# Performance work log

Measured on AMD Instinct MI355X. Metric: run time of the kernel, lower is better.

Reference implementation:

```python
import jax, jax.numpy as jnp
import numpy as np

LN_EPS = 1e-5

def _pos_enc(S, d):
    # sinusoid table; row 0 is all zeros (matches position_encoding_init)
    j = np.arange(d)
    pos = np.arange(S, dtype=np.float64)[:, None]
    pe = pos / np.power(10000.0, 2 * (j // 2) / d)
    pe[0, :] = 0.0
    pe[1:, 0::2] = np.sin(pe[1:, 0::2])
    pe[1:, 1::2] = np.cos(pe[1:, 1::2])
    return jnp.asarray(pe, dtype=jnp.float32)


def setup_inputs() -> dict:
    key = jax.random.key(0)
    ks = jax.random.split(key, 8)
    B, S, din, dhid = 8, 2048, 1024, 1024
    inp = jax.random.normal(ks[0], (B, S, din), dtype=jnp.float32)
    lens = jax.random.randint(ks[1], (B,), 1, S, dtype=jnp.int64)
    scale = 0.02
    Wq = jax.random.normal(ks[2], (2 * din, dhid), dtype=jnp.float32) * scale
    Wk = jax.random.normal(ks[3], (2 * din, dhid), dtype=jnp.float32) * scale
    Wv = jax.random.normal(ks[4], (2 * din, dhid), dtype=jnp.float32) * scale
    bq = jax.random.normal(ks[5], (dhid,), dtype=jnp.float32) * scale
    bk = jax.random.normal(ks[6], (dhid,), dtype=jnp.float32) * scale
    bv = jax.random.normal(ks[7], (dhid,), dtype=jnp.float32) * scale
    gamma = jnp.ones((dhid,), dtype=jnp.float32)
    beta = jnp.zeros((dhid,), dtype=jnp.float32)
    return {"inp": inp, "Wq": Wq, "bq": bq, "Wk": Wk, "bk": bk,
            "Wv": Wv, "bv": bv, "gamma": gamma, "beta": beta, "lens": lens}


def reference(inp, Wq, bq, Wk, bk, Wv, bv, gamma, beta, lens):
    B, S, d = inp.shape
    pe = _pos_enc(S, d)  # [S, d], static given shapes
    x = jnp.concatenate([inp, jnp.broadcast_to(pe, (B, S, d))], axis=-1)  # [B,S,2d]
    q = x @ Wq + bq  # [B,S,dk]
    k = x @ Wk + bk
    v = x @ Wv + bv
    scores = jnp.einsum('bqd,bkd->bqk', q, k)  # [B,S,S]
    # NOTE: softmax over the QUERY axis (dim=1), then post-hoc scale, as in the source
    attn = jax.nn.softmax(scores, axis=1) / jnp.sqrt(jnp.asarray(q.shape[-1], jnp.float32))
    sa = jnp.einsum('bqk,bkd->bqd', attn, v)  # [B,S,dv]
    mu = sa.mean(axis=-1, keepdims=True)
    var = sa.var(axis=-1, keepdims=True)
    ln = (sa - mu) / jnp.sqrt(var + LN_EPS) * gamma + beta
    context = ln.sum(axis=1) / S  # [B,dv]
    return (sa, context)
```

## Files before the change

kernel.cpp:

```cpp
#include <hip/hip_runtime.h>
#include <math.h>

#define B_   8
#define S_   2048
#define D_   1024
#define M_   (B_ * S_)
#define K2_  (2 * D_)


__global__ __launch_bounds__(256) void pe_fill(float* __restrict__ pe) {
    const int s  = blockIdx.x;
    const int j0 = threadIdx.x * 4;
#pragma unroll
    for (int e = 0; e < 4; ++e) {
        int j = j0 + e;
        double ex = (double)(2 * (j >> 1)) / (double)D_;
        double dv = pow(10000.0, ex);
        double a  = (double)s / dv;
        float val;
        if (s == 0) val = 0.0f;
        else        val = (j & 1) ? (float)cos(a) : (float)sin(a);
        pe[s * D_ + j] = val;
    }
}


__device__ __forceinline__ void stage_trans(const float* __restrict__ src,
                                            int ld, int row0, int k0,
                                            float (*T)[132], int tid) {
#pragma unroll
    for (int it = 0; it < 2; ++it) {
        int f  = tid + it * 256;
        int r  = f >> 2;
        int c4 = (f & 3) << 2;
        float4 v = *(const float4*)&src[(size_t)(row0 + r) * ld + k0 + c4];
        T[c4 + 0][r] = v.x;
        T[c4 + 1][r] = v.y;
        T[c4 + 2][r] = v.z;
        T[c4 + 3][r] = v.w;
    }
}

__device__ __forceinline__ void stage_direct(const float* __restrict__ src,
                                             int ld, int k0, int col0,
                                             float (*T)[132], int tid) {
#pragma unroll
    for (int it = 0; it < 2; ++it) {
        int f  = tid + it * 256;
        int kr = f >> 5;
        int c4 = (f & 31) << 2;
        float4 v = *(const float4*)&src[(size_t)(k0 + kr) * ld + col0 + c4];
        *(float4*)&T[kr][c4] = v;
    }
}

__device__ __forceinline__ void mm_core(const float (*As)[132],
                                        const float (*Bs)[132],
                                        float acc[8][8], int tx, int ty) {
#pragma unroll
    for (int kk = 0; kk < 16; ++kk) {
        float a[8], b[8];
        *(float4*)&a[0] = *(const float4*)&As[kk][ty * 8];
        *(float4*)&a[4] = *(const float4*)&As[kk][ty * 8 + 4];
        *(float4*)&b[0] = *(const float4*)&Bs[kk][tx * 8];
        *(float4*)&b[4] = *(const float4*)&Bs[kk][tx * 8 + 4];
#pragma unroll
        for (int i = 0; i < 8; ++i)
#pragma unroll
            for (int j = 0; j < 8; ++j)
                acc[i][j] = fmaf(a[i], b[j], acc[i][j]);
    }
}

__global__ __launch_bounds__(256) void proj_gemm(
        const float* __restrict__ inp, const float* __restrict__ pe,
        const float* __restrict__ W, const float* __restrict__ bias,
        float* __restrict__ out, int m_base) {
    __shared__ float As[16][132];
    __shared__ float Bs[16][132];
    const int tid = threadIdx.x;
    const int tx = tid & 15, ty = tid >> 4;
    const int m0 = blockIdx.x * 128;
    const int n0 = blockIdx.y * 128;

    float acc[8][8];
#pragma unroll
    for (int i = 0; i < 8; ++i)
#pragma unroll
        for (int j = 0; j < 8; ++j) acc[i][j] = 0.0f;

    for (int k0 = 0; k0 < K2_; k0 += 16) {
#pragma unroll
        for (int it = 0; it < 2; ++it) {
            int f  = tid + it * 256;
            int r  = f >> 2;
            int c4 = (f & 3) << 2;
            int gm = m_base + m0 + r;
            float4 v;
            if (k0 < D_) {
                v = *(const float4*)&inp[(size_t)gm * D_ + k0 + c4];
            } else {
                int s = gm & (S_ - 1);
                v = *(const float4*)&pe[(size_t)s * D_ + (k0 - D_) + c4];
            }
            As[c4 + 0][r] = v.x;
            As[c4 + 1][r] = v.y;
            As[c4 + 2][r] = v.z;
            As[c4 + 3][r] = v.w;
        }
        stage_direct(W, D_, k0, n0, Bs, tid);
        __syncthreads();
        mm_core(As, Bs, acc, tx, ty);
        __syncthreads();
    }

    float bv[8];
    *(float4*)&bv[0] = *(const float4*)&bias[n0 + tx * 8];
    *(float4*)&bv[4] = *(const float4*)&bias[n0 + tx * 8 + 4];
#pragma unroll
    for (int i = 0; i < 8; ++i) {
        int m = m0 + ty * 8 + i;
        float o[8];
#pragma unroll
        for (int j = 0; j < 8; ++j) o[j] = acc[i][j] + bv[j];
        *(float4*)&out[(size_t)m * D_ + n0 + tx * 8]     = *(float4*)&o[0];
        *(float4*)&out[(size_t)m * D_ + n0 + tx * 8 + 4] = *(float4*)&o[4];
    }
}

__global__ __launch_bounds__(256) void qk_gemm(
        const float* __restrict__ q, const float* __restrict__ k,
        float* __restrict__ scoresT) {
    __shared__ float As[16][132];
    __shared__ float Bs[16][132];
    const int tid = threadIdx.x;
    const int tx = tid & 15, ty = tid >> 4;
    const int b  = blockIdx.z;
    const int i0 = blockIdx.x * 128;
    const int j0 = blockIdx.y * 128;
    const float* Kb = k + (size_t)b * S_ * D_;
    const float* Qb = q + (size_t)b * S_ * D_;

    float acc[8][8];
#pragma unroll
    for (int i = 0; i < 8; ++i)
#pragma unroll
        for (int j = 0; j < 8; ++j) acc[i][j] = 0.0f;

    for (int d0 = 0; d0 < D_; d0 += 16) {
        stage_trans(Kb, D_, i0, d0, As, tid);
        stage_trans(Qb, D_, j0, d0, Bs, tid);
        __syncthreads();
        mm_core(As, Bs, acc, tx, ty);
        __syncthreads();
    }

    float* outb = scoresT + (size_t)b * S_ * S_;
#pragma unroll
    for (int i = 0; i < 8; ++i) {
        int ii = i0 + ty * 8 + i;
        *(float4*)&outb[(size_t)ii * S_ + j0 + tx * 8]     = *(float4*)&acc[i][0];
        *(float4*)&outb[(size_t)ii * S_ + j0 + tx * 8 + 4] = *(float4*)&acc[i][4];
    }
}

__global__ __launch_bounds__(256) void softmax_rows(float* __restrict__ scoresT) {
    const size_t row = blockIdx.x;
    float* p = scoresT + row * S_;
    const int tid = threadIdx.x;

    __shared__ float sm[4], ss[4];

    float4 x0 = *(const float4*)&p[tid * 4];
    float4 x1 = *(const float4*)&p[1024 + tid * 4];

    float mx = fmaxf(fmaxf(fmaxf(x0.x, x0.y), fmaxf(x0.z, x0.w)),
                     fmaxf(fmaxf(x1.x, x1.y), fmaxf(x1.z, x1.w)));
#pragma unroll
    for (int o = 32; o > 0; o >>= 1) mx = fmaxf(mx, __shfl_xor(mx, o));
    if ((tid & 63) == 0) sm[tid >> 6] = mx;
    __syncthreads();
    mx = fmaxf(fmaxf(sm[0], sm[1]), fmaxf(sm[2], sm[3]));

    float e[8];
    e[0] = expf(x0.x - mx); e[1] = expf(x0.y - mx);
    e[2] = expf(x0.z - mx); e[3] = expf(x0.w - mx);
    e[4] = expf(x1.x - mx); e[5] = expf(x1.y - mx);
    e[6] = expf(x1.z - mx); e[7] = expf(x1.w - mx);
    float s = e[0] + e[1] + e[2] + e[3] + e[4] + e[5] + e[6] + e[7];
#pragma unroll
    for (int o = 32; o > 0; o >>= 1) s += __shfl_xor(s, o);
    if ((tid & 63) == 0) ss[tid >> 6] = s;
    __syncthreads();
    s = ss[0] + ss[1] + ss[2] + ss[3];

    const float sc = 0.03125f / s;
    float4 o0 = make_float4(e[0] * sc, e[1] * sc, e[2] * sc, e[3] * sc);
    float4 o1 = make_float4(e[4] * sc, e[5] * sc, e[6] * sc, e[7] * sc);
    *(float4*)&p[tid * 4]        = o0;
    *(float4*)&p[1024 + tid * 4] = o1;
}

__global__ __launch_bounds__(256) void av_gemm(
        const float* __restrict__ P, const float* __restrict__ V,
        float* __restrict__ sa) {
    __shared__ float As[16][132];
    __shared__ float Bs[16][132];
    const int tid = threadIdx.x;
    const int tx = tid & 15, ty = tid >> 4;
    const int b  = blockIdx.z;
    const int q0 = blockIdx.x * 128;
    const int n0 = blockIdx.y * 128;
    const float* Pb = P + (size_t)b * S_ * S_;
    const float* Vb = V + (size_t)b * S_ * D_;

    float acc[8][8];
#pragma unroll
    for (int i = 0; i < 8; ++i)
#pragma unroll
        for (int j = 0; j < 8; ++j) acc[i][j] = 0.0f;

    for (int k0 = 0; k0 < S_; k0 += 16) {
        stage_direct(Pb, S_, k0, q0, As, tid);
        stage_direct(Vb, D_, k0, n0, Bs, tid);
        __syncthreads();
        mm_core(As, Bs, acc, tx, ty);
        __syncthreads();
    }

    float* outb = sa + (size_t)b * S_ * D_;
#pragma unroll
    for (int i = 0; i < 8; ++i) {
        int qq = q0 + ty * 8 + i;
        *(float4*)&outb[(size_t)qq * D_ + n0 + tx * 8]     = *(float4*)&acc[i][0];
        *(float4*)&outb[(size_t)qq * D_ + n0 + tx * 8 + 4] = *(float4*)&acc[i][4];
    }
}

__global__ __launch_bounds__(256) void zero_f(float* __restrict__ p, int n) {
    int i = blockIdx.x * 256 + threadIdx.x;
    if (i < n) p[i] = 0.0f;
}

__global__ __launch_bounds__(256) void ln_ctx(
        const float* __restrict__ sa, const float* __restrict__ gamma,
        const float* __restrict__ beta, float* __restrict__ ctx) {
    const int blk = blockIdx.x;
    const int b   = blk >> 4;
    const int r0  = (blk & 15) * 128;
    const int tid = threadIdx.x;
    const int c   = tid * 4;

    __shared__ float sred[8];

    float g[4], be[4];
    *(float4*)&g[0]  = *(const float4*)&gamma[c];
    *(float4*)&be[0] = *(const float4*)&beta[c];

    float accv[4] = {0.0f, 0.0f, 0.0f, 0.0f};

    for (int r = 0; r < 128; ++r) {
        const float* row = sa + (size_t)(b * S_ + r0 + r) * D_;
        float x[4];
        *(float4*)&x[0] = *(const float4*)&row[c];
        float s  = x[0] + x[1] + x[2] + x[3];
        float s2 = fmaf(x[0], x[0], fmaf(x[1], x[1], fmaf(x[2], x[2], x[3] * x[3])));
#pragma unroll
        for (int o = 32; o > 0; o >>= 1) {
            s  += __shfl_xor(s, o);
            s2 += __shfl_xor(s2, o);
        }
        if ((tid & 63) == 0) { sred[tid >> 6] = s; sred[4 + (tid >> 6)] = s2; }
        __syncthreads();
        float sum   = sred[0] + sred[1] + sred[2] + sred[3];
        float sumsq = sred[4] + sred[5] + sred[6] + sred[7];
        __syncthreads();

        float mu  = sum * (1.0f / (float)D_);
        float var = sumsq * (1.0f / (float)D_) - mu * mu;
        float rs  = rsqrtf(var + 1e-5f);
#pragma unroll
        for (int j = 0; j < 4; ++j)
            accv[j] += (x[j] - mu) * rs * g[j] + be[j];
    }

#pragma unroll
    for (int j = 0; j < 4; ++j)
        atomicAdd(&ctx[b * D_ + c + j], accv[j] * (1.0f / (float)S_));
}

extern "C" void kernel_launch(void* const* d_in, const int* in_sizes, int n_in,
                              void* d_out, int out_size, void* d_ws, size_t ws_size,
                              hipStream_t stream) {
    const float* inp   = (const float*)d_in[0];
    const float* Wq    = (const float*)d_in[1];
    const float* bq    = (const float*)d_in[2];
    const float* Wk    = (const float*)d_in[3];
    const float* bk    = (const float*)d_in[4];
    const float* Wv    = (const float*)d_in[5];
    const float* bv    = (const float*)d_in[6];
    const float* gamma = (const float*)d_in[7];
    const float* beta  = (const float*)d_in[8];

    const size_t MiB = 1024 * 1024;
    int c = 1;
    if      (ws_size >= 8 * MiB + 8 * 32 * MiB) c = 8;
    else if (ws_size >= 8 * MiB + 4 * 32 * MiB) c = 4;
    else if (ws_size >= 8 * MiB + 2 * 32 * MiB) c = 2;

    float* ws      = (float*)d_ws;
    float* pe      = ws;
    float* bufQV   = pe + (size_t)S_ * D_;
    float* bufK    = bufQV + (size_t)c * S_ * D_;
    float* scoresT = bufK  + (size_t)c * S_ * D_;

    float* sa  = (float*)d_out;
    float* ctx = (float*)d_out + (size_t)M_ * D_;

    pe_fill<<<dim3(S_), dim3(256), 0, stream>>>(pe);

    const int nchunk = B_ / c;
    for (int ch = 0; ch < nchunk; ++ch) {
        const int b0     = ch * c;
        const int m_base = b0 * S_;

        proj_gemm<<<dim3(16 * c, 8), dim3(256), 0, stream>>>(inp, pe, Wq, bq, bufQV, m_base);
        proj_gemm<<<dim3(16 * c, 8), dim3(256), 0, stream>>>(inp, pe, Wk, bk, bufK,  m_base);

        qk_gemm<<<dim3(16, 16, c), dim3(256), 0, stream>>>(bufQV, bufK, scoresT);

        softmax_rows<<<dim3(c * S_), dim3(256), 0, stream>>>(scoresT);

        proj_gemm<<<dim3(16 * c, 8), dim3(256), 0, stream>>>(inp, pe, Wv, bv, bufQV, m_base);

        av_gemm<<<dim3(16, 8, c), dim3(256), 0, stream>>>(scoresT, bufQV,
                                                          sa + (size_t)b0 * S_ * D_);
    }

    zero_f<<<dim3(32), dim3(256), 0, stream>>>(ctx, B_ * D_);
    ln_ctx<<<dim3(128), dim3(256), 0, stream>>>(sa, gamma, beta, ctx);
}
```

Before: 4.577 ms.

## Double GEMM K-tile, interleave thread fragments, widen LN grid, cheaper PE

The shared-memory K-tile for all GEMMs grows from 16 to 32, halving the number of barrier-separated iterations. Each thread's 8x8 micro-tile is split into two strided 4-wide halves (rows/cols t*4 and 64+t*4), which reduces LDS bank conflicts on float4 reads. The LayerNorm/context reduction kernel now uses 1024 blocks of 16 rows instead of 128 blocks of 128 rows for more parallelism, at the cost of more atomic contention on ctx. The positional-encoding fill replaces pow with exp2, which can change results slightly.

```diff
diff --git a/kernel.cpp b/kernel.cpp
--- a/kernel.cpp
+++ b/kernel.cpp
@@ -6,17 +6,18 @@
 #define D_   1024
 #define M_   (B_ * S_)
 #define K2_  (2 * D_)
+#define BK   32
 
 
 __global__ __launch_bounds__(256) void pe_fill(float* __restrict__ pe) {
     const int s  = blockIdx.x;
     const int j0 = threadIdx.x * 4;
+    const double L2_1E4 = 13.287712379549449;
 #pragma unroll
     for (int e = 0; e < 4; ++e) {
         int j = j0 + e;
         double ex = (double)(2 * (j >> 1)) / (double)D_;
-        double dv = pow(10000.0, ex);
-        double a  = (double)s / dv;
+        double a  = (double)s * exp2(-ex * L2_1E4);
         float val;
         if (s == 0) val = 0.0f;
         else        val = (j & 1) ? (float)cos(a) : (float)sin(a);
@@ -29,10 +30,10 @@
                                             int ld, int row0, int k0,
                                             float (*T)[132], int tid) {
 #pragma unroll
-    for (int it = 0; it < 2; ++it) {
+    for (int it = 0; it < 4; ++it) {
         int f  = tid + it * 256;
-        int r  = f >> 2;
-        int c4 = (f & 3) << 2;
+        int r  = f >> 3;
+        int c4 = (f & 7) << 2;
         float4 v = *(const float4*)&src[(size_t)(row0 + r) * ld + k0 + c4];
         T[c4 + 0][r] = v.x;
         T[c4 + 1][r] = v.y;
@@ -45,7 +46,7 @@
                                              int ld, int k0, int col0,
                                              float (*T)[132], int tid) {
 #pragma unroll
-    for (int it = 0; it < 2; ++it) {
+    for (int it = 0; it < 4; ++it) {
         int f  = tid + it * 256;
         int kr = f >> 5;
         int c4 = (f & 31) << 2;
@@ -58,26 +59,30 @@
                                         const float (*Bs)[132],
                                         float acc[8][8], int tx, int ty) {
 #pragma unroll
-    for (int kk = 0; kk < 16; ++kk) {
+    for (int kk = 0; kk < BK; ++kk) {
         float a[8], b[8];
-        *(float4*)&a[0] = *(const float4*)&As[kk][ty * 8];
-        *(float4*)&a[4] = *(const float4*)&As[kk][ty * 8 + 4];
-        *(float4*)&b[0] = *(const float4*)&Bs[kk][tx * 8];
-        *(float4*)&b[4] = *(const float4*)&Bs[kk][tx * 8 + 4];
+        *(float4*)&a[0] = *(const float4*)&As[kk][ty * 4];
+        *(float4*)&a[4] = *(const float4*)&As[kk][64 + ty * 4];
+        *(float4*)&b[0] = *(const float4*)&Bs[kk][tx * 4];
+        *(float4*)&b[4] = *(const float4*)&Bs[kk][64 + tx * 4];
 #pragma unroll
         for (int i = 0; i < 8; ++i)
 #pragma unroll
             for (int j = 0; j < 8; ++j)
                 acc[i][j] = fmaf(a[i], b[j], acc[i][j]);
     }
+}
+
+__device__ __forceinline__ int frag_idx(int t4, int h, int e) {
+    return h == 0 ? t4 * 4 + e : 64 + t4 * 4 + e;
 }
 
 __global__ __launch_bounds__(256) void proj_gemm(
         const float* __restrict__ inp, const float* __restrict__ pe,
         const float* __restrict__ W, const float* __restrict__ bias,
         float* __restrict__ out, int m_base) {
-    __shared__ float As[16][132];
-    __shared__ float Bs[16][132];
+    __shared__ float As[BK][132];
+    __shared__ float Bs[BK][132];
     const int tid = threadIdx.x;
     const int tx = tid & 15, ty = tid >> 4;
     const int m0 = blockIdx.x * 128;
@@ -89,12 +94,12 @@
 #pragma unroll
         for (int j = 0; j < 8; ++j) acc[i][j] = 0.0f;
 
-    for (int k0 = 0; k0 < K2_; k0 += 16) {
-#pragma unroll
-        for (int it = 0; it < 2; ++it) {
+    for (int k0 = 0; k0 < K2_; k0 += BK) {
+#pragma unroll
+        for (int it = 0; it < 4; ++it) {
             int f  = tid + it * 256;
-            int r  = f >> 2;
-            int c4 = (f & 3) << 2;
+            int r  = f >> 3;
+            int c4 = (f & 7) << 2;
             int gm = m_base + m0 + r;
             float4 v;
             if (k0 < D_) {
@@ -115,24 +120,27 @@
     }
 
     float bv[8];
-    *(float4*)&bv[0] = *(const float4*)&bias[n0 + tx * 8];
-    *(float4*)&bv[4] = *(const float4*)&bias[n0 + tx * 8 + 4];
-#pragma unroll
-    for (int i = 0; i < 8; ++i) {
-        int m = m0 + ty * 8 + i;
+    *(float4*)&bv[0] = *(const float4*)&bias[n0 + tx * 4];
+    *(float4*)&bv[4] = *(const float4*)&bias[n0 + 64 + tx * 4];
+#pragma unroll
+    for (int ih = 0; ih < 2; ++ih)
+#pragma unroll
+    for (int ii = 0; ii < 4; ++ii) {
+        int i = ih * 4 + ii;
+        int m = m0 + frag_idx(ty, ih, ii);
         float o[8];
 #pragma unroll
         for (int j = 0; j < 8; ++j) o[j] = acc[i][j] + bv[j];
-        *(float4*)&out[(size_t)m * D_ + n0 + tx * 8]     = *(float4*)&o[0];
-        *(float4*)&out[(size_t)m * D_ + n0 + tx * 8 + 4] = *(float4*)&o[4];
+        *(float4*)&out[(size_t)m * D_ + n0 + tx * 4]      = *(float4*)&o[0];
+        *(float4*)&out[(size_t)m * D_ + n0 + 64 + tx * 4] = *(float4*)&o[4];
     }
 }
 
 __global__ __launch_bounds__(256) void qk_gemm(
         const float* __restrict__ q, const float* __restrict__ k,
         float* __restrict__ scoresT) {
-    __shared__ float As[16][132];
-    __shared__ float Bs[16][132];
+    __shared__ float As[BK][132];
+    __shared__ float Bs[BK][132];
     const int tid = threadIdx.x;
     const int tx = tid & 15, ty = tid >> 4;
     const int b  = blockIdx.z;
@@ -147,7 +155,7 @@
 #pragma unroll
         for (int j = 0; j < 8; ++j) acc[i][j] = 0.0f;
 
-    for (int d0 = 0; d0 < D_; d0 += 16) {
+    for (int d0 = 0; d0 < D_; d0 += BK) {
         stage_trans(Kb, D_, i0, d0, As, tid);
         stage_trans(Qb, D_, j0, d0, Bs, tid);
         __syncthreads();
@@ -157,10 +165,13 @@
 
     float* outb = scoresT + (size_t)b * S_ * S_;
 #pragma unroll
-    for (int i = 0; i < 8; ++i) {
-        int ii = i0 + ty * 8 + i;
-        *(float4*)&outb[(size_t)ii * S_ + j0 + tx * 8]     = *(float4*)&acc[i][0];
-        *(float4*)&outb[(size_t)ii * S_ + j0 + tx * 8 + 4] = *(float4*)&acc[i][4];
+    for (int ih = 0; ih < 2; ++ih)
+#pragma unroll
+    for (int ii = 0; ii < 4; ++ii) {
+        int i  = ih * 4 + ii;
+        int ir = i0 + frag_idx(ty, ih, ii);
+        *(float4*)&outb[(size_t)ir * S_ + j0 + tx * 4]      = *(float4*)&acc[i][0];
+        *(float4*)&outb[(size_t)ir * S_ + j0 + 64 + tx * 4] = *(float4*)&acc[i][4];
     }
 }
 
@@ -204,8 +215,8 @@
 __global__ __launch_bounds__(256) void av_gemm(
         const float* __restrict__ P, const float* __restrict__ V,
         float* __restrict__ sa) {
-    __shared__ float As[16][132];
-    __shared__ float Bs[16][132];
+    __shared__ float As[BK][132];
+    __shared__ float Bs[BK][132];
     const int tid = threadIdx.x;
     const int tx = tid & 15, ty = tid >> 4;
     const int b  = blockIdx.z;
@@ -220,7 +231,7 @@
 #pragma unroll
         for (int j = 0; j < 8; ++j) acc[i][j] = 0.0f;
 
-    for (int k0 = 0; k0 < S_; k0 += 16) {
+    for (int k0 = 0; k0 < S_; k0 += BK) {
         stage_direct(Pb, S_, k0, q0, As, tid);
         stage_direct(Vb, D_, k0, n0, Bs, tid);
         __syncthreads();
@@ -230,10 +241,13 @@
 
     float* outb = sa + (size_t)b * S_ * D_;
 #pragma unroll
-    for (int i = 0; i < 8; ++i) {
-        int qq = q0 + ty * 8 + i;
-        *(float4*)&outb[(size_t)qq * D_ + n0 + tx * 8]     = *(float4*)&acc[i][0];
-        *(float4*)&outb[(size_t)qq * D_ + n0 + tx * 8 + 4] = *(float4*)&acc[i][4];
+    for (int ih = 0; ih < 2; ++ih)
+#pragma unroll
+    for (int ii = 0; ii < 4; ++ii) {
+        int i  = ih * 4 + ii;
+        int qq = q0 + frag_idx(ty, ih, ii);
+        *(float4*)&outb[(size_t)qq * D_ + n0 + tx * 4]      = *(float4*)&acc[i][0];
+        *(float4*)&outb[(size_t)qq * D_ + n0 + 64 + tx * 4] = *(float4*)&acc[i][4];
     }
 }
 
@@ -245,11 +259,10 @@
 __global__ __launch_bounds__(256) void ln_ctx(
         const float* __restrict__ sa, const float* __restrict__ gamma,
         const float* __restrict__ beta, float* __restrict__ ctx) {
-    const int blk = blockIdx.x;
-    const int b   = blk >> 4;
-    const int r0  = (blk & 15) * 128;
-    const int tid = threadIdx.x;
-    const int c   = tid * 4;
+    const int row0 = blockIdx.x * 16;
+    const int b    = row0 >> 11;
+    const int tid  = threadIdx.x;
+    const int c    = tid * 4;
 
     __shared__ float sred[8];
 
@@ -259,8 +272,8 @@
 
     float accv[4] = {0.0f, 0.0f, 0.0f, 0.0f};
 
-    for (int r = 0; r < 128; ++r) {
-        const float* row = sa + (size_t)(b * S_ + r0 + r) * D_;
+    for (int r = 0; r < 16; ++r) {
+        const float* row = sa + (size_t)(row0 + r) * D_;
         float x[4];
         *(float4*)&x[0] = *(const float4*)&row[c];
         float s  = x[0] + x[1] + x[2] + x[3];
@@ -338,5 +351,5 @@
     }
 
     zero_f<<<dim3(32), dim3(256), 0, stream>>>(ctx, B_ * D_);
-    ln_ctx<<<dim3(128), dim3(256), 0, stream>>>(sa, gamma, beta, ctx);
-}
+    ln_ctx<<<dim3(1024), dim3(256), 0, stream>>>(sa, gamma, beta, ctx);
+}
```

After: 4.236 ms. -7.5%, faster.
